# Optimization experiments

Measured on AMD Instinct MI355X. Metric: run time of the kernel, lower is better.

## Reference

```python
import jax, jax.numpy as jnp
import numpy as np
import math

B, S, D, H, DH, R = 2, 2048, 1024, 16, 64, 8
EPS = 1e-5


def setup_inputs() -> dict:
    key = jax.random.key(0)
    ks = jax.random.split(key, 8)
    hidden_states = jax.random.normal(ks[0], (B, S, D), jnp.float32)
    # causal boolean mask (batch, seq, seq); every row has >=1 valid entry
    causal = jnp.tril(jnp.ones((S, S), dtype=bool))
    attention_mask = jnp.broadcast_to(causal, (B, S, S))
    # lora: (n_layers=1, 4, batch, hidden, rank); [0]=qA,[1]=kA,[2]=qB,[3]=kB
    lora = jax.random.normal(ks[1], (1, 4, B, D, R), jnp.float32) * 0.02
    ln_w = jnp.ones((D,), jnp.float32)
    Wq = jax.random.normal(ks[2], (D, D), jnp.float32) * 0.02
    Wk = jax.random.normal(ks[3], (D, D), jnp.float32) * 0.02
    Wv = jax.random.normal(ks[4], (D, D), jnp.float32) * 0.02
    Wo = jax.random.normal(ks[5], (D, D), jnp.float32) * 0.02
    return dict(hidden_states=hidden_states, attention_mask=attention_mask,
                lora=lora, ln_w=ln_w, Wq=Wq, Wk=Wk, Wv=Wv, Wo=Wo)


def _rms_ln(x, w):
    # model_center LayerNorm with bias=False == RMS layernorm
    var = jnp.mean(x * x, axis=-1, keepdims=True)
    return x * jax.lax.rsqrt(var + EPS) * w


def _lora_delta(h, A, Bm):
    # h: (b,s,D), A: (b,D,R), Bm: (b,R,D);  h + (h@A)@Bm * 2
    z = jnp.einsum('bsd,bdr->bsr', h, A)
    return h + jnp.einsum('bsr,brd->bsd', z, Bm) * 2


def reference(hidden_states, attention_mask, lora, ln_w, Wq, Wk, Wv, Wo):
    b, s, _ = hidden_states.shape
    x = _rms_ln(hidden_states, ln_w)
    h_q = x @ Wq.T
    h_k = x @ Wk.T
    h_v = x @ Wv.T
    layer = lora[0]  # (4, b, D, R)
    h_q = _lora_delta(h_q, layer[0], jnp.swapaxes(layer[2], 1, 2))
    h_k = _lora_delta(h_k, layer[1], jnp.swapaxes(layer[3], 1, 2))
    q = h_q.reshape(b, s, H, DH)
    k = h_k.reshape(b, s, H, DH)
    v = h_v.reshape(b, s, H, DH)
    score = jnp.einsum('bqhd,bkhd->bhqk', q, k) / math.sqrt(DH)
    m = attention_mask[:, None, :, :]  # (b,1,s,s)
    score = jnp.where(m, score, -jnp.inf)
    p = jax.nn.softmax(score, axis=-1)
    p = jnp.where(m, p, jnp.float32(0))
    out = jnp.einsum('bhqk,bkhd->bqhd', p, v).reshape(b, s, H * DH)
    out = out @ Wo.T
    return hidden_states + out
```

## Files before the change

kernel.cpp:

```cpp
#include <hip/hip_runtime.h>

typedef __bf16 bf16;
typedef __bf16 bf16x4 __attribute__((ext_vector_type(4)));
typedef __bf16 bf16x8 __attribute__((ext_vector_type(8)));
typedef float f32x4 __attribute__((ext_vector_type(4)));

#define DM 1024
#define NROW 4096
#define SEQ 2048
#define HDIM 64
#define NEGBIG -30000.0f

#define SWB(base, row, bcol) \
  ((char*)(base) + (row) * 128 + ((bcol) ^ (((row) & 7) << 4)))

__device__ __forceinline__ void async16(const bf16* g, bf16* l) {
  __builtin_amdgcn_global_load_lds(
      (const __attribute__((address_space(1))) unsigned int*)g,
      (__attribute__((address_space(3))) unsigned int*)l, 16, 0, 0);
}

template <bool F32OUT>
__device__ __forceinline__ void gemm128(const bf16* __restrict__ A,
                                        const bf16* __restrict__ Bw,
                                        bf16* __restrict__ Cb,
                                        float* __restrict__ Cf,
                                        const float* __restrict__ resid,
                                        int m0, int n0) {
  __shared__ __align__(16) bf16 sA[128 * 32];
  __shared__ __align__(16) bf16 sB[128 * 32];
  const int t = threadIdx.x;
  const int lane = t & 63;
  const int w = t >> 6;
  const int wm = (w & 1) * 64;
  const int wn = (w >> 1) * 64;
  const int lr = lane & 15;
  const int kg = lane >> 4;

  f32x4 acc[4][4];
#pragma unroll
  for (int i = 0; i < 4; i++)
#pragma unroll
    for (int j = 0; j < 4; j++)
#pragma unroll
      for (int r = 0; r < 4; r++) acc[i][j][r] = 0.0f;

  const int srow = t >> 2;
  const int scol = (t & 3) * 8;
  const bf16* gA = A + (size_t)(m0 + srow) * DM + scol;
  const bf16* gB = Bw + (size_t)(n0 + srow) * DM + scol;
  bf16* lA = &sA[t * 8];
  bf16* lB = &sB[t * 8];

  for (int k0 = 0; k0 < DM; k0 += 32) {
    async16(gA + k0, lA);
    async16(gA + k0 + 64 * DM, lA + 2048);
    async16(gB + k0, lB);
    async16(gB + k0 + 64 * DM, lB + 2048);
    __syncthreads();
    bf16x8 av[4], bv[4];
#pragma unroll
    for (int mi = 0; mi < 4; mi++)
      av[mi] = *(const bf16x8*)&sA[(wm + mi * 16 + lr) * 32 + kg * 8];
#pragma unroll
    for (int nj = 0; nj < 4; nj++)
      bv[nj] = *(const bf16x8*)&sB[(wn + nj * 16 + lr) * 32 + kg * 8];
#pragma unroll
    for (int mi = 0; mi < 4; mi++)
#pragma unroll
      for (int nj = 0; nj < 4; nj++)
        acc[mi][nj] = __builtin_amdgcn_mfma_f32_16x16x32_bf16(av[mi], bv[nj],
                                                              acc[mi][nj], 0, 0, 0);
    __syncthreads();
  }

#pragma unroll
  for (int mi = 0; mi < 4; mi++) {
#pragma unroll
    for (int r = 0; r < 4; r++) {
      const int grow = m0 + wm + mi * 16 + kg * 4 + r;
      const size_t base = (size_t)grow * DM + n0 + wn + lr;
#pragma unroll
      for (int nj = 0; nj < 4; nj++) {
        float v = acc[mi][nj][r];
        if (F32OUT) {
          Cf[base + nj * 16] = v + resid[base + nj * 16];
        } else {
          Cb[base + nj * 16] = (bf16)v;
        }
      }
    }
  }
}

__global__ __launch_bounds__(256) void k_cast4(const float* __restrict__ a,
                                               const float* __restrict__ b,
                                               const float* __restrict__ c,
                                               const float* __restrict__ e,
                                               bf16* __restrict__ d) {
  const int i = blockIdx.x * 256 + threadIdx.x;
  const int mat = i >> 18;
  const int off = i & 262143;
  const float* s = (mat == 0) ? a : (mat == 1) ? b : (mat == 2) ? c : e;
  const float4 v = ((const float4*)s)[off];
  bf16x4 o;
  o[0] = (bf16)v.x; o[1] = (bf16)v.y; o[2] = (bf16)v.z; o[3] = (bf16)v.w;
  ((bf16x4*)d)[i] = o;
}

__global__ __launch_bounds__(256) void k_rmsnorm(const float* __restrict__ hin,
                                                 const float* __restrict__ wln,
                                                 bf16* __restrict__ xo) {
  const int row = blockIdx.x;
  const int t = threadIdx.x;
  const float4 h4 = ((const float4*)(hin + (size_t)row * DM))[t];
  float ss = h4.x * h4.x + h4.y * h4.y + h4.z * h4.z + h4.w * h4.w;
#pragma unroll
  for (int off = 1; off < 64; off <<= 1) ss += __shfl_xor(ss, off, 64);
  __shared__ float red[4];
  if ((t & 63) == 0) red[t >> 6] = ss;
  __syncthreads();
  ss = red[0] + red[1] + red[2] + red[3];
  const float inv = rsqrtf(ss * (1.0f / DM) + 1e-5f);
  const float4 w4 = ((const float4*)wln)[t];
  bf16x4 o;
  o[0] = (bf16)(h4.x * inv * w4.x);
  o[1] = (bf16)(h4.y * inv * w4.y);
  o[2] = (bf16)(h4.z * inv * w4.z);
  o[3] = (bf16)(h4.w * inv * w4.w);
  *(bf16x4*)&xo[(size_t)row * DM + t * 4] = o;
}

__global__ __launch_bounds__(256) void k_qkv(const bf16* __restrict__ x,
                                             const bf16* __restrict__ Wq,
                                             const bf16* __restrict__ Wk,
                                             const bf16* __restrict__ Wv,
                                             bf16* __restrict__ hq,
                                             bf16* __restrict__ hk,
                                             bf16* __restrict__ hv) {
  const int nb = blockIdx.y;
  const int wsel = nb >> 3;
  const int n0 = (nb & 7) * 128;
  const bf16* Bw = (wsel == 0) ? Wq : (wsel == 1) ? Wk : Wv;
  bf16* C = (wsel == 0) ? hq : (wsel == 1) ? hk : hv;
  gemm128<false>(x, Bw, C, nullptr, nullptr, blockIdx.x * 128, n0);
}

__global__ __launch_bounds__(256) void k_oproj(const bf16* __restrict__ ctx,
                                               const bf16* __restrict__ Wo,
                                               const float* __restrict__ resid,
                                               float* __restrict__ out) {
  gemm128<true>(ctx, Wo, nullptr, out, resid, blockIdx.x * 128, blockIdx.y * 128);
}

__global__ __launch_bounds__(256) void k_vt(const bf16* __restrict__ hv,
                                            bf16* __restrict__ hvT) {
  __shared__ __align__(16) bf16 sT[64 * 64];
  const int t = threadIdx.x;
  const int s0 = blockIdx.x * 64;
  const int c0 = blockIdx.y * 64;
  const int b = blockIdx.z;
  const int r = t >> 2;
  const int cc = (t & 3) * 16;
  const bf16* g = hv + ((size_t)(b * SEQ + s0 + r)) * DM + c0 + cc;
  const bf16x8 a0 = *(const bf16x8*)g;
  const bf16x8 a1 = *(const bf16x8*)(g + 8);
  *(bf16x8*)SWB(sT, r, cc * 2) = a0;
  *(bf16x8*)SWB(sT, r, cc * 2 + 16) = a1;
  __syncthreads();
  bf16x8 o0, o1;
#pragma unroll
  for (int j = 0; j < 8; j++) {
    o0[j] = *(const bf16*)SWB(sT, cc + j, r * 2);
    o1[j] = *(const bf16*)SWB(sT, cc + 8 + j, r * 2);
  }
  bf16* o = hvT + ((size_t)(b * DM + c0 + r)) * SEQ + s0 + cc;
  *(bf16x8*)o = o0;
  *(bf16x8*)(o + 8) = o1;
}

__global__ __launch_bounds__(256) void k_lora2(bf16* __restrict__ hq,
                                               bf16* __restrict__ hk,
                                               const float* __restrict__ lora) {
  const int row0 = blockIdx.x * 32;
  const int which = blockIdx.y;
  const int b = row0 >> 11;
  bf16* H = (which == 0 ? hq : hk) + (size_t)row0 * DM;
  const float* Am = lora + (size_t)(which == 0 ? 0 : 1) * 16384 + (size_t)b * 8192;
  const float* Bm = lora + (size_t)(which == 0 ? 2 : 3) * 16384 + (size_t)b * 8192;
  const int t = threadIdx.x;
  const int lane = t & 63;
  const int w = t >> 6;
  const int lr = lane & 15;
  const int kg = lane >> 4;

  __shared__ __align__(16) bf16 At[8 * 1024];
  __shared__ float Zp[2][32][8];

  const int d0 = lane * 16;
  float4 Bv[32];
  {
    const float4* bp = (const float4*)(Bm + (size_t)d0 * 8);
#pragma unroll
    for (int i = 0; i < 32; i++) Bv[i] = bp[i];
  }

  {
    const float4* ap = (const float4*)(Am + (size_t)t * 32);
#pragma unroll
    for (int i = 0; i < 8; i++) {
      const float4 v = ap[i];
      const int idx = t * 32 + i * 4;
      At[(idx & 7) * 1024 + (idx >> 3)]             = (bf16)v.x;
      At[((idx + 1) & 7) * 1024 + ((idx + 1) >> 3)] = (bf16)v.y;
      At[((idx + 2) & 7) * 1024 + ((idx + 2) >> 3)] = (bf16)v.z;
      At[((idx + 3) & 7) * 1024 + ((idx + 3) >> 3)] = (bf16)v.w;
    }
  }
  __syncthreads();

  const int tile = w & 1;
  const int khalf = w >> 1;
  {
    f32x4 zacc;
#pragma unroll
    for (int r = 0; r < 4; r++) zacc[r] = 0.f;
    const bf16* gH = H + (size_t)(tile * 16 + lr) * DM + khalf * 512 + kg * 8;
    const bf16* lA = &At[(lr & 7) * 1024 + khalf * 512 + kg * 8];
#pragma unroll
    for (int i = 0; i < 16; i++) {
      const bf16x8 ah = *(const bf16x8*)(gH + i * 32);
      const bf16x8 ba = *(const bf16x8*)(lA + i * 32);
      zacc = __builtin_amdgcn_mfma_f32_16x16x32_bf16(ah, ba, zacc, 0, 0, 0);
    }
    if (lr < 8) {
#pragma unroll
      for (int r = 0; r < 4; r++) Zp[khalf][tile * 16 + kg * 4 + r][lr] = zacc[r];
    }
  }
  __syncthreads();

#pragma unroll
  for (int rr = 0; rr < 8; rr++) {
    const int row = w * 8 + rr;
    const float4 z0 = *(const float4*)&Zp[0][row][0];
    const float4 z1 = *(const float4*)&Zp[0][row][4];
    const float4 y0 = *(const float4*)&Zp[1][row][0];
    const float4 y1 = *(const float4*)&Zp[1][row][4];
    const float za = z0.x + y0.x, zb = z0.y + y0.y, zc = z0.z + y0.z, zd = z0.w + y0.w;
    const float ze = z1.x + y1.x, zf = z1.y + y1.y, zg = z1.z + y1.z, zh = z1.w + y1.w;
    bf16* hp = H + (size_t)row * DM + d0;
    const bf16x8 h0 = *(const bf16x8*)hp;
    const bf16x8 h1 = *(const bf16x8*)(hp + 8);
    bf16x8 o0, o1;
#pragma unroll
    for (int j = 0; j < 16; j++) {
      const float4 b0 = Bv[2 * j];
      const float4 b1 = Bv[2 * j + 1];
      const float delta = za * b0.x + zb * b0.y + zc * b0.z + zd * b0.w +
                          ze * b1.x + zf * b1.y + zg * b1.z + zh * b1.w;
      const float hj = (j < 8) ? (float)h0[j] : (float)h1[j - 8];
      const bf16 ov = (bf16)(hj + 2.0f * delta);
      if (j < 8) o0[j] = ov; else o1[j - 8] = ov;
    }
    *(bf16x8*)hp = o0;
    *(bf16x8*)(hp + 8) = o1;
  }
}

__global__ __launch_bounds__(256, 4) void k_attn(const bf16* __restrict__ hq,
                                                 const bf16* __restrict__ hk,
                                                 const bf16* __restrict__ hvT,
                                                 bf16* __restrict__ ctx) {
  const int n = blockIdx.x;
  const int slab = n & 31;
  const int hh = slab & 15;
  const int b = slab >> 4;
  const int xx = n >> 5;
  const int s = xx >> 3;
  const int v = xx & 7;
  const int qt = (s == 0) ? 4 * v : (s == 1) ? 31 - 4 * v
               : (s == 2) ? 4 * v + 2 : 29 - 4 * v;
  const int qbase = qt * 64;

  const int t = threadIdx.x;
  const int lane = t & 63;
  const int w = t >> 6;
  const int lr = lane & 15;
  const int kg = lane >> 4;

  __shared__ __align__(16) bf16 sQ[64 * 64];
  __shared__ __align__(16) bf16 sK[64 * 64];
  __shared__ __align__(16) bf16 sVt[64 * 64];
  __shared__ __align__(16) bf16 sP[64 * 64];

  const size_t rowbase = (size_t)b * SEQ;
  const int hoff = hh * HDIM;
  const float sscale = 0.18033688011112042f;

  const int r4 = t >> 2;
  const int ce = (t & 3) * 16;
  const int cb = (t & 3) * 32;

  {
    const bf16* g = hq + (rowbase + qbase + r4) * DM + hoff + ce;
    bf16x8 q0 = *(const bf16x8*)g;
    bf16x8 q1 = *(const bf16x8*)(g + 8);
    bf16x8 o0, o1;
#pragma unroll
    for (int j = 0; j < 8; j++) {
      o0[j] = (bf16)((float)q0[j] * sscale);
      o1[j] = (bf16)((float)q1[j] * sscale);
    }
    *(bf16x8*)SWB(sQ, r4, cb) = o0;
    *(bf16x8*)SWB(sQ, r4, cb + 16) = o1;
  }

  const bf16* gK = hk + (rowbase + r4) * DM + hoff + ce;
  const bf16* gV = hvT + ((size_t)slab * HDIM + r4) * SEQ + ce;
  bf16x8 kr0 = *(const bf16x8*)gK;
  bf16x8 kr1 = *(const bf16x8*)(gK + 8);
  bf16x8 vr0 = *(const bf16x8*)gV;
  bf16x8 vr1 = *(const bf16x8*)(gV + 8);

  float m_l = NEGBIG, l_l = 0.f;
  f32x4 oacc[4];
#pragma unroll
  for (int nj = 0; nj < 4; nj++)
#pragma unroll
    for (int r = 0; r < 4; r++) oacc[nj][r] = 0.f;

  __syncthreads();

  for (int kt = 0; kt <= qt; kt++) {
    *(bf16x8*)SWB(sK, r4, cb) = kr0;
    *(bf16x8*)SWB(sK, r4, cb + 16) = kr1;
    *(bf16x8*)SWB(sVt, r4, cb) = vr0;
    *(bf16x8*)SWB(sVt, r4, cb + 16) = vr1;
    __syncthreads();

    if (kt < qt) {
      const bf16* gK2 = gK + (size_t)(kt + 1) * 64 * DM;
      const bf16* gV2 = gV + (kt + 1) * 64;
      kr0 = *(const bf16x8*)gK2;
      kr1 = *(const bf16x8*)(gK2 + 8);
      vr0 = *(const bf16x8*)gV2;
      vr1 = *(const bf16x8*)(gV2 + 8);
    }

    f32x4 sc[4];
#pragma unroll
    for (int nj = 0; nj < 4; nj++)
#pragma unroll
      for (int r = 0; r < 4; r++) sc[nj][r] = 0.f;
#pragma unroll
    for (int ks = 0; ks < 2; ks++) {
      const bf16x8 bq = *(const bf16x8*)SWB(sQ, w * 16 + lr, ks * 64 + kg * 16);
#pragma unroll
      for (int nj = 0; nj < 4; nj++) {
        const bf16x8 ak = *(const bf16x8*)SWB(sK, nj * 16 + lr, ks * 64 + kg * 16);
        sc[nj] = __builtin_amdgcn_mfma_f32_16x16x32_bf16(ak, bq, sc[nj], 0, 0, 0);
      }
    }

    if (kt == qt) {
      const int ql = w * 16 + lr;
#pragma unroll
      for (int nj = 0; nj < 4; nj++)
#pragma unroll
        for (int r = 0; r < 4; r++) {
          const int kl = nj * 16 + kg * 4 + r;
          sc[nj][r] = (kl <= ql) ? sc[nj][r] : NEGBIG;
        }
    }

    float rm = sc[0][0];
#pragma unroll
    for (int nj = 0; nj < 4; nj++)
#pragma unroll
      for (int r = 0; r < 4; r++) rm = fmaxf(rm, sc[nj][r]);
    rm = fmaxf(rm, __shfl_xor(rm, 16, 64));
    rm = fmaxf(rm, __shfl_xor(rm, 32, 64));
    const float mnew = fmaxf(m_l, rm);
    const float alpha = __builtin_amdgcn_exp2f(m_l - mnew);
    float rs = 0.f;
#pragma unroll
    for (int nj = 0; nj < 4; nj++)
#pragma unroll
      for (int r = 0; r < 4; r++) {
        const float p = __builtin_amdgcn_exp2f(sc[nj][r] - mnew);
        sc[nj][r] = p;
        rs += p;
      }
    rs += __shfl_xor(rs, 16, 64);
    rs += __shfl_xor(rs, 32, 64);
    l_l = l_l * alpha + rs;
    m_l = mnew;

#pragma unroll
    for (int nj = 0; nj < 4; nj++) {
      bf16x4 p4;
#pragma unroll
      for (int r = 0; r < 4; r++) p4[r] = (bf16)sc[nj][r];
      *(bf16x4*)SWB(sP, w * 16 + lr, nj * 32 + kg * 8) = p4;
    }

#pragma unroll
    for (int r = 0; r < 4; r++) {
      const float ar = __shfl(alpha, (lane & 48) | (kg * 4 + r), 64);
#pragma unroll
      for (int nj = 0; nj < 4; nj++) oacc[nj][r] *= ar;
    }

#pragma unroll
    for (int ks = 0; ks < 2; ks++) {
      const bf16x8 ap = *(const bf16x8*)SWB(sP, w * 16 + lr, ks * 64 + kg * 16);
#pragma unroll
      for (int nj = 0; nj < 4; nj++) {
        const bf16x8 bv = *(const bf16x8*)SWB(sVt, nj * 16 + lr, ks * 64 + kg * 16);
        oacc[nj] = __builtin_amdgcn_mfma_f32_16x16x32_bf16(ap, bv, oacc[nj], 0, 0, 0);
      }
    }
    __syncthreads();
  }

#pragma unroll
  for (int r = 0; r < 4; r++) {
    const float lrow = __shfl(l_l, (lane & 48) | (kg * 4 + r), 64);
    const float invl = 1.0f / lrow;
    const int qr = qbase + w * 16 + kg * 4 + r;
    const size_t base = (rowbase + qr) * DM + hoff + lr;
#pragma unroll
    for (int nj = 0; nj < 4; nj++)
      ctx[base + nj * 16] = (bf16)(oacc[nj][r] * invl);
  }
}

extern "C" void kernel_launch(void* const* d_in, const int* in_sizes, int n_in,
                              void* d_out, int out_size, void* d_ws, size_t ws_size,
                              hipStream_t stream) {
  const float* hidden = (const float*)d_in[0];
  const float* lora = (const float*)d_in[2];
  const float* wln  = (const float*)d_in[3];
  const float* Wq   = (const float*)d_in[4];
  const float* Wk   = (const float*)d_in[5];
  const float* Wv   = (const float*)d_in[6];
  const float* Wo   = (const float*)d_in[7];
  float* out = (float*)d_out;

  const size_t BUF = (size_t)NROW * DM;
  if (ws_size < 4 * BUF * sizeof(bf16)) return;
  bf16* ws = (bf16*)d_ws;
  bf16* hq  = ws;
  bf16* hk  = ws + 1 * BUF;
  bf16* hv  = ws + 2 * BUF;
  bf16* ctx = ws + 3 * BUF;

  bf16* dob = (bf16*)d_out;
  bf16* x   = dob;
  bf16* wqb = dob + BUF;
  bf16* wkb = dob + BUF + DM * DM;
  bf16* wvb = dob + BUF + 2 * DM * DM;
  bf16* wob = dob + BUF + 3 * DM * DM;
  bf16* hvT = dob;

  k_cast4<<<dim3(4 * 1024), dim3(256), 0, stream>>>(Wq, Wk, Wv, Wo, wqb);
  k_rmsnorm<<<dim3(NROW), dim3(256), 0, stream>>>(hidden, wln, x);
  k_qkv<<<dim3(32, 24), dim3(256), 0, stream>>>(x, wqb, wkb, wvb, hq, hk, hv);
  k_vt<<<dim3(SEQ / 64, DM / 64, 2), dim3(256), 0, stream>>>(hv, hvT);
  k_lora2<<<dim3(128, 2), dim3(256), 0, stream>>>(hq, hk, lora);
  k_attn<<<dim3(1024), dim3(256), 0, stream>>>(hq, hk, hvT, ctx);
  k_oproj<<<dim3(32, 8), dim3(256), 0, stream>>>(ctx, wob, hidden, out);
}
```

Measured before the change: 222.0 us.

## Merge small kernels and double-buffer attention K/V with async LDS loads

Merges the weight-cast and RMSnorm kernels into one launch, and the V-transpose and LoRA kernels into another, cutting launch count and tail gaps. In the attention kernel, K and V tiles are now double-buffered in LDS and fetched with global_load_lds async copies issued one tile ahead, in place of the register staging and extra LDS store pass. MFMA sections are wrapped in s_setprio, and the launch-bounds occupancy hint drops from 4 to 3 to make room for the larger LDS footprint. The async loads use an XOR-swizzled layout that has to match the SWB read pattern, and the extra LDS per block may lower occupancy.

Measured after the change: 226.8 us. +2.2%, slower.

```diff
diff --git a/kernel.cpp b/kernel.cpp
--- a/kernel.cpp
+++ b/kernel.cpp
@@ -93,42 +93,44 @@
   }
 }
 
-__global__ __launch_bounds__(256) void k_cast4(const float* __restrict__ a,
-                                               const float* __restrict__ b,
-                                               const float* __restrict__ c,
-                                               const float* __restrict__ e,
-                                               bf16* __restrict__ d) {
-  const int i = blockIdx.x * 256 + threadIdx.x;
-  const int mat = i >> 18;
-  const int off = i & 262143;
-  const float* s = (mat == 0) ? a : (mat == 1) ? b : (mat == 2) ? c : e;
-  const float4 v = ((const float4*)s)[off];
-  bf16x4 o;
-  o[0] = (bf16)v.x; o[1] = (bf16)v.y; o[2] = (bf16)v.z; o[3] = (bf16)v.w;
-  ((bf16x4*)d)[i] = o;
-}
-
-__global__ __launch_bounds__(256) void k_rmsnorm(const float* __restrict__ hin,
-                                                 const float* __restrict__ wln,
-                                                 bf16* __restrict__ xo) {
-  const int row = blockIdx.x;
+__global__ __launch_bounds__(256) void k_pre(const float* __restrict__ hin,
+                                             const float* __restrict__ wln,
+                                             const float* __restrict__ Wq,
+                                             const float* __restrict__ Wk,
+                                             const float* __restrict__ Wv,
+                                             const float* __restrict__ Wo,
+                                             bf16* __restrict__ xo,
+                                             bf16* __restrict__ wcast) {
+  __shared__ float red[4];
   const int t = threadIdx.x;
-  const float4 h4 = ((const float4*)(hin + (size_t)row * DM))[t];
-  float ss = h4.x * h4.x + h4.y * h4.y + h4.z * h4.z + h4.w * h4.w;
-#pragma unroll
-  for (int off = 1; off < 64; off <<= 1) ss += __shfl_xor(ss, off, 64);
-  __shared__ float red[4];
-  if ((t & 63) == 0) red[t >> 6] = ss;
-  __syncthreads();
-  ss = red[0] + red[1] + red[2] + red[3];
-  const float inv = rsqrtf(ss * (1.0f / DM) + 1e-5f);
-  const float4 w4 = ((const float4*)wln)[t];
-  bf16x4 o;
-  o[0] = (bf16)(h4.x * inv * w4.x);
-  o[1] = (bf16)(h4.y * inv * w4.y);
-  o[2] = (bf16)(h4.z * inv * w4.z);
-  o[3] = (bf16)(h4.w * inv * w4.w);
-  *(bf16x4*)&xo[(size_t)row * DM + t * 4] = o;
+  const int bb = blockIdx.x;
+  if (bb < NROW) {
+    const int row = bb;
+    const float4 h4 = ((const float4*)(hin + (size_t)row * DM))[t];
+    float ss = h4.x * h4.x + h4.y * h4.y + h4.z * h4.z + h4.w * h4.w;
+#pragma unroll
+    for (int off = 1; off < 64; off <<= 1) ss += __shfl_xor(ss, off, 64);
+    if ((t & 63) == 0) red[t >> 6] = ss;
+    __syncthreads();
+    ss = red[0] + red[1] + red[2] + red[3];
+    const float inv = rsqrtf(ss * (1.0f / DM) + 1e-5f);
+    const float4 w4 = ((const float4*)wln)[t];
+    bf16x4 o;
+    o[0] = (bf16)(h4.x * inv * w4.x);
+    o[1] = (bf16)(h4.y * inv * w4.y);
+    o[2] = (bf16)(h4.z * inv * w4.z);
+    o[3] = (bf16)(h4.w * inv * w4.w);
+    *(bf16x4*)&xo[(size_t)row * DM + t * 4] = o;
+  } else {
+    const int i = (bb - NROW) * 256 + t;
+    const int mat = i >> 18;
+    const int off = i & 262143;
+    const float* s = (mat == 0) ? Wq : (mat == 1) ? Wk : (mat == 2) ? Wv : Wo;
+    const float4 v = ((const float4*)s)[off];
+    bf16x4 o;
+    o[0] = (bf16)v.x; o[1] = (bf16)v.y; o[2] = (bf16)v.z; o[3] = (bf16)v.w;
+    ((bf16x4*)wcast)[i] = o;
+  }
 }
 
 __global__ __launch_bounds__(256) void k_qkv(const bf16* __restrict__ x,
@@ -153,122 +155,126 @@
   gemm128<true>(ctx, Wo, nullptr, out, resid, blockIdx.x * 128, blockIdx.y * 128);
 }
 
-__global__ __launch_bounds__(256) void k_vt(const bf16* __restrict__ hv,
-                                            bf16* __restrict__ hvT) {
-  __shared__ __align__(16) bf16 sT[64 * 64];
+__global__ __launch_bounds__(256) void k_mid(const bf16* __restrict__ hv,
+                                             bf16* __restrict__ hvT,
+                                             bf16* __restrict__ hq,
+                                             bf16* __restrict__ hk,
+                                             const float* __restrict__ lora) {
+  __shared__ __align__(16) char smem[18432];
   const int t = threadIdx.x;
-  const int s0 = blockIdx.x * 64;
-  const int c0 = blockIdx.y * 64;
-  const int b = blockIdx.z;
-  const int r = t >> 2;
-  const int cc = (t & 3) * 16;
-  const bf16* g = hv + ((size_t)(b * SEQ + s0 + r)) * DM + c0 + cc;
-  const bf16x8 a0 = *(const bf16x8*)g;
-  const bf16x8 a1 = *(const bf16x8*)(g + 8);
-  *(bf16x8*)SWB(sT, r, cc * 2) = a0;
-  *(bf16x8*)SWB(sT, r, cc * 2 + 16) = a1;
-  __syncthreads();
-  bf16x8 o0, o1;
-#pragma unroll
-  for (int j = 0; j < 8; j++) {
-    o0[j] = *(const bf16*)SWB(sT, cc + j, r * 2);
-    o1[j] = *(const bf16*)SWB(sT, cc + 8 + j, r * 2);
-  }
-  bf16* o = hvT + ((size_t)(b * DM + c0 + r)) * SEQ + s0 + cc;
-  *(bf16x8*)o = o0;
-  *(bf16x8*)(o + 8) = o1;
-}
-
-__global__ __launch_bounds__(256) void k_lora2(bf16* __restrict__ hq,
-                                               bf16* __restrict__ hk,
-                                               const float* __restrict__ lora) {
-  const int row0 = blockIdx.x * 32;
-  const int which = blockIdx.y;
-  const int b = row0 >> 11;
-  bf16* H = (which == 0 ? hq : hk) + (size_t)row0 * DM;
-  const float* Am = lora + (size_t)(which == 0 ? 0 : 1) * 16384 + (size_t)b * 8192;
-  const float* Bm = lora + (size_t)(which == 0 ? 2 : 3) * 16384 + (size_t)b * 8192;
-  const int t = threadIdx.x;
+  const int bb = blockIdx.x;
   const int lane = t & 63;
   const int w = t >> 6;
   const int lr = lane & 15;
   const int kg = lane >> 4;
 
-  __shared__ __align__(16) bf16 At[8 * 1024];
-  __shared__ float Zp[2][32][8];
-
-  const int d0 = lane * 16;
-  float4 Bv[32];
-  {
-    const float4* bp = (const float4*)(Bm + (size_t)d0 * 8);
-#pragma unroll
-    for (int i = 0; i < 32; i++) Bv[i] = bp[i];
-  }
-
-  {
-    const float4* ap = (const float4*)(Am + (size_t)t * 32);
-#pragma unroll
-    for (int i = 0; i < 8; i++) {
-      const float4 v = ap[i];
-      const int idx = t * 32 + i * 4;
-      At[(idx & 7) * 1024 + (idx >> 3)]             = (bf16)v.x;
-      At[((idx + 1) & 7) * 1024 + ((idx + 1) >> 3)] = (bf16)v.y;
-      At[((idx + 2) & 7) * 1024 + ((idx + 2) >> 3)] = (bf16)v.z;
-      At[((idx + 3) & 7) * 1024 + ((idx + 3) >> 3)] = (bf16)v.w;
-    }
-  }
-  __syncthreads();
-
-  const int tile = w & 1;
-  const int khalf = w >> 1;
-  {
-    f32x4 zacc;
-#pragma unroll
-    for (int r = 0; r < 4; r++) zacc[r] = 0.f;
-    const bf16* gH = H + (size_t)(tile * 16 + lr) * DM + khalf * 512 + kg * 8;
-    const bf16* lA = &At[(lr & 7) * 1024 + khalf * 512 + kg * 8];
-#pragma unroll
-    for (int i = 0; i < 16; i++) {
-      const bf16x8 ah = *(const bf16x8*)(gH + i * 32);
-      const bf16x8 ba = *(const bf16x8*)(lA + i * 32);
-      zacc = __builtin_amdgcn_mfma_f32_16x16x32_bf16(ah, ba, zacc, 0, 0, 0);
-    }
-    if (lr < 8) {
-#pragma unroll
-      for (int r = 0; r < 4; r++) Zp[khalf][tile * 16 + kg * 4 + r][lr] = zacc[r];
-    }
-  }
-  __syncthreads();
-
-#pragma unroll
-  for (int rr = 0; rr < 8; rr++) {
-    const int row = w * 8 + rr;
-    const float4 z0 = *(const float4*)&Zp[0][row][0];
-    const float4 z1 = *(const float4*)&Zp[0][row][4];
-    const float4 y0 = *(const float4*)&Zp[1][row][0];
-    const float4 y1 = *(const float4*)&Zp[1][row][4];
-    const float za = z0.x + y0.x, zb = z0.y + y0.y, zc = z0.z + y0.z, zd = z0.w + y0.w;
-    const float ze = z1.x + y1.x, zf = z1.y + y1.y, zg = z1.z + y1.z, zh = z1.w + y1.w;
-    bf16* hp = H + (size_t)row * DM + d0;
-    const bf16x8 h0 = *(const bf16x8*)hp;
-    const bf16x8 h1 = *(const bf16x8*)(hp + 8);
+  if (bb < 1024) {
+    bf16* sT = (bf16*)smem;
+    const int s0 = (bb & 31) * 64;
+    const int c0 = ((bb >> 5) & 15) * 64;
+    const int b = bb >> 9;
+    const int r = t >> 2;
+    const int cc = (t & 3) * 16;
+    const bf16* g = hv + ((size_t)(b * SEQ + s0 + r)) * DM + c0 + cc;
+    const bf16x8 a0 = *(const bf16x8*)g;
+    const bf16x8 a1 = *(const bf16x8*)(g + 8);
+    *(bf16x8*)SWB(sT, r, cc * 2) = a0;
+    *(bf16x8*)SWB(sT, r, cc * 2 + 16) = a1;
+    __syncthreads();
     bf16x8 o0, o1;
 #pragma unroll
-    for (int j = 0; j < 16; j++) {
-      const float4 b0 = Bv[2 * j];
-      const float4 b1 = Bv[2 * j + 1];
-      const float delta = za * b0.x + zb * b0.y + zc * b0.z + zd * b0.w +
-                          ze * b1.x + zf * b1.y + zg * b1.z + zh * b1.w;
-      const float hj = (j < 8) ? (float)h0[j] : (float)h1[j - 8];
-      const bf16 ov = (bf16)(hj + 2.0f * delta);
-      if (j < 8) o0[j] = ov; else o1[j - 8] = ov;
-    }
-    *(bf16x8*)hp = o0;
-    *(bf16x8*)(hp + 8) = o1;
-  }
-}
-
-__global__ __launch_bounds__(256, 4) void k_attn(const bf16* __restrict__ hq,
+    for (int j = 0; j < 8; j++) {
+      o0[j] = *(const bf16*)SWB(sT, cc + j, r * 2);
+      o1[j] = *(const bf16*)SWB(sT, cc + 8 + j, r * 2);
+    }
+    bf16* o = hvT + ((size_t)(b * DM + c0 + r)) * SEQ + s0 + cc;
+    *(bf16x8*)o = o0;
+    *(bf16x8*)(o + 8) = o1;
+  } else {
+    bf16* At = (bf16*)smem;
+    float* Zp = (float*)(smem + 16384);
+    const int lid = bb - 1024;
+    const int row0 = (lid & 127) * 32;
+    const int which = lid >> 7;
+    const int b = row0 >> 11;
+    bf16* H = (which == 0 ? hq : hk) + (size_t)row0 * DM;
+    const float* Am = lora + (size_t)(which == 0 ? 0 : 1) * 16384 + (size_t)b * 8192;
+    const float* Bm = lora + (size_t)(which == 0 ? 2 : 3) * 16384 + (size_t)b * 8192;
+
+    const int d0 = lane * 16;
+    float4 Bv[32];
+    {
+      const float4* bp = (const float4*)(Bm + (size_t)d0 * 8);
+#pragma unroll
+      for (int i = 0; i < 32; i++) Bv[i] = bp[i];
+    }
+
+    {
+      const float4* ap = (const float4*)(Am + (size_t)t * 32);
+#pragma unroll
+      for (int i = 0; i < 8; i++) {
+        const float4 v = ap[i];
+        const int idx = t * 32 + i * 4;
+        At[(idx & 7) * 1024 + (idx >> 3)]             = (bf16)v.x;
+        At[((idx + 1) & 7) * 1024 + ((idx + 1) >> 3)] = (bf16)v.y;
+        At[((idx + 2) & 7) * 1024 + ((idx + 2) >> 3)] = (bf16)v.z;
+        At[((idx + 3) & 7) * 1024 + ((idx + 3) >> 3)] = (bf16)v.w;
+      }
+    }
+    __syncthreads();
+
+    const int tile = w & 1;
+    const int khalf = w >> 1;
+    {
+      f32x4 zacc;
+#pragma unroll
+      for (int r = 0; r < 4; r++) zacc[r] = 0.f;
+      const bf16* gH = H + (size_t)(tile * 16 + lr) * DM + khalf * 512 + kg * 8;
+      const bf16* lA = &At[(lr & 7) * 1024 + khalf * 512 + kg * 8];
+#pragma unroll
+      for (int i = 0; i < 16; i++) {
+        const bf16x8 ah = *(const bf16x8*)(gH + i * 32);
+        const bf16x8 ba = *(const bf16x8*)(lA + i * 32);
+        zacc = __builtin_amdgcn_mfma_f32_16x16x32_bf16(ah, ba, zacc, 0, 0, 0);
+      }
+      if (lr < 8) {
+#pragma unroll
+        for (int r = 0; r < 4; r++)
+          Zp[(khalf * 32 + tile * 16 + kg * 4 + r) * 8 + lr] = zacc[r];
+      }
+    }
+    __syncthreads();
+
+#pragma unroll
+    for (int rr = 0; rr < 8; rr++) {
+      const int row = w * 8 + rr;
+      const float4 z0 = *(const float4*)&Zp[(row) * 8 + 0];
+      const float4 z1 = *(const float4*)&Zp[(row) * 8 + 4];
+      const float4 y0 = *(const float4*)&Zp[(32 + row) * 8 + 0];
+      const float4 y1 = *(const float4*)&Zp[(32 + row) * 8 + 4];
+      const float za = z0.x + y0.x, zb = z0.y + y0.y, zc = z0.z + y0.z, zd = z0.w + y0.w;
+      const float ze = z1.x + y1.x, zf = z1.y + y1.y, zg = z1.z + y1.z, zh = z1.w + y1.w;
+      bf16* hp = H + (size_t)row * DM + d0;
+      const bf16x8 h0 = *(const bf16x8*)hp;
+      const bf16x8 h1 = *(const bf16x8*)(hp + 8);
+      bf16x8 o0, o1;
+#pragma unroll
+      for (int j = 0; j < 16; j++) {
+        const float4 b0 = Bv[2 * j];
+        const float4 b1 = Bv[2 * j + 1];
+        const float delta = za * b0.x + zb * b0.y + zc * b0.z + zd * b0.w +
+                            ze * b1.x + zf * b1.y + zg * b1.z + zh * b1.w;
+        const float hj = (j < 8) ? (float)h0[j] : (float)h1[j - 8];
+        const bf16 ov = (bf16)(hj + 2.0f * delta);
+        if (j < 8) o0[j] = ov; else o1[j - 8] = ov;
+      }
+      *(bf16x8*)hp = o0;
+      *(bf16x8*)(hp + 8) = o1;
+    }
+  }
+}
+
+__global__ __launch_bounds__(256, 3) void k_attn(const bf16* __restrict__ hq,
                                                  const bf16* __restrict__ hk,
                                                  const bf16* __restrict__ hvT,
                                                  bf16* __restrict__ ctx) {
@@ -290,19 +296,18 @@
   const int kg = lane >> 4;
 
   __shared__ __align__(16) bf16 sQ[64 * 64];
-  __shared__ __align__(16) bf16 sK[64 * 64];
-  __shared__ __align__(16) bf16 sVt[64 * 64];
+  __shared__ __align__(16) bf16 sK[2][64 * 64];
+  __shared__ __align__(16) bf16 sVt[2][64 * 64];
   __shared__ __align__(16) bf16 sP[64 * 64];
 
   const size_t rowbase = (size_t)b * SEQ;
   const int hoff = hh * HDIM;
   const float sscale = 0.18033688011112042f;
 
-  const int r4 = t >> 2;
-  const int ce = (t & 3) * 16;
-  const int cb = (t & 3) * 32;
-
   {
+    const int r4 = t >> 2;
+    const int ce = (t & 3) * 16;
+    const int cb = (t & 3) * 32;
     const bf16* g = hq + (rowbase + qbase + r4) * DM + hoff + ce;
     bf16x8 q0 = *(const bf16x8*)g;
     bf16x8 q1 = *(const bf16x8*)(g + 8);
@@ -316,12 +321,27 @@
     *(bf16x8*)SWB(sQ, r4, cb + 16) = o1;
   }
 
-  const bf16* gK = hk + (rowbase + r4) * DM + hoff + ce;
-  const bf16* gV = hvT + ((size_t)slab * HDIM + r4) * SEQ + ce;
-  bf16x8 kr0 = *(const bf16x8*)gK;
-  bf16x8 kr1 = *(const bf16x8*)(gK + 8);
-  bf16x8 vr0 = *(const bf16x8*)gV;
-  bf16x8 vr1 = *(const bf16x8*)(gV + 8);
+  const int l3 = lane >> 3;
+  const int dcol = ((lane & 7) ^ l3) * 8;
+  const int drow = w * 16 + l3;
+  const bf16* gKb = hk + (rowbase + drow) * DM + hoff + dcol;
+  const bf16* gVb = hvT + ((size_t)slab * HDIM + drow) * SEQ + dcol;
+  bf16* lK = &sK[0][0] + w * 1024 + lane * 8;
+  bf16* lV = &sVt[0][0] + w * 1024 + lane * 8;
+
+#define ISSUE_KV(kt_, buf_)                                          \
+  {                                                                  \
+    const bf16* gk_ = gKb + (size_t)(kt_) * 64 * DM;                 \
+    const bf16* gv_ = gVb + (kt_) * 64;                              \
+    bf16* lk_ = lK + (buf_) * 4096;                                  \
+    bf16* lv_ = lV + (buf_) * 4096;                                  \
+    async16(gk_, lk_);                                               \
+    async16(gk_ + 8 * DM, lk_ + 512);                                \
+    async16(gv_, lv_);                                               \
+    async16(gv_ + 8 * SEQ, lv_ + 512);                               \
+  }
+
+  ISSUE_KV(0, 0);
 
   float m_l = NEGBIG, l_l = 0.f;
   f32x4 oacc[4];
@@ -330,38 +350,31 @@
 #pragma unroll
     for (int r = 0; r < 4; r++) oacc[nj][r] = 0.f;
 
+  asm volatile("s_waitcnt vmcnt(0)" ::: "memory");
   __syncthreads();
 
   for (int kt = 0; kt <= qt; kt++) {
-    *(bf16x8*)SWB(sK, r4, cb) = kr0;
-    *(bf16x8*)SWB(sK, r4, cb + 16) = kr1;
-    *(bf16x8*)SWB(sVt, r4, cb) = vr0;
-    *(bf16x8*)SWB(sVt, r4, cb + 16) = vr1;
-    __syncthreads();
-
-    if (kt < qt) {
-      const bf16* gK2 = gK + (size_t)(kt + 1) * 64 * DM;
-      const bf16* gV2 = gV + (kt + 1) * 64;
-      kr0 = *(const bf16x8*)gK2;
-      kr1 = *(const bf16x8*)(gK2 + 8);
-      vr0 = *(const bf16x8*)gV2;
-      vr1 = *(const bf16x8*)(gV2 + 8);
-    }
+    const int cur = kt & 1;
+    if (kt < qt) ISSUE_KV(kt + 1, cur ^ 1);
+    const bf16* sKc = &sK[cur][0];
+    const bf16* sVc = &sVt[cur][0];
 
     f32x4 sc[4];
 #pragma unroll
     for (int nj = 0; nj < 4; nj++)
 #pragma unroll
       for (int r = 0; r < 4; r++) sc[nj][r] = 0.f;
+    __builtin_amdgcn_s_setprio(1);
 #pragma unroll
     for (int ks = 0; ks < 2; ks++) {
       const bf16x8 bq = *(const bf16x8*)SWB(sQ, w * 16 + lr, ks * 64 + kg * 16);
 #pragma unroll
       for (int nj = 0; nj < 4; nj++) {
-        const bf16x8 ak = *(const bf16x8*)SWB(sK, nj * 16 + lr, ks * 64 + kg * 16);
+        const bf16x8 ak = *(const bf16x8*)SWB(sKc, nj * 16 + lr, ks * 64 + kg * 16);
         sc[nj] = __builtin_amdgcn_mfma_f32_16x16x32_bf16(ak, bq, sc[nj], 0, 0, 0);
       }
     }
+    __builtin_amdgcn_s_setprio(0);
 
     if (kt == qt) {
       const int ql = w * 16 + lr;
@@ -412,15 +425,19 @@
       for (int nj = 0; nj < 4; nj++) oacc[nj][r] *= ar;
     }
 
+    __builtin_amdgcn_s_setprio(1);
 #pragma unroll
     for (int ks = 0; ks < 2; ks++) {
       const bf16x8 ap = *(const bf16x8*)SWB(sP, w * 16 + lr, ks * 64 + kg * 16);
 #pragma unroll
       for (int nj = 0; nj < 4; nj++) {
-        const bf16x8 bv = *(const bf16x8*)SWB(sVt, nj * 16 + lr, ks * 64 + kg * 16);
+        const bf16x8 bv = *(const bf16x8*)SWB(sVc, nj * 16 + lr, ks * 64 + kg * 16);
         oacc[nj] = __builtin_amdgcn_mfma_f32_16x16x32_bf16(ap, bv, oacc[nj], 0, 0, 0);
       }
     }
+    __builtin_amdgcn_s_setprio(0);
+
+    asm volatile("s_waitcnt vmcnt(0)" ::: "memory");
     __syncthreads();
   }
 
@@ -464,11 +481,9 @@
   bf16* wob = dob + BUF + 3 * DM * DM;
   bf16* hvT = dob;
 
-  k_cast4<<<dim3(4 * 1024), dim3(256), 0, stream>>>(Wq, Wk, Wv, Wo, wqb);
-  k_rmsnorm<<<dim3(NROW), dim3(256), 0, stream>>>(hidden, wln, x);
+  k_pre<<<dim3(2 * NROW), dim3(256), 0, stream>>>(hidden, wln, Wq, Wk, Wv, Wo, x, wqb);
   k_qkv<<<dim3(32, 24), dim3(256), 0, stream>>>(x, wqb, wkb, wvb, hq, hk, hv);
-  k_vt<<<dim3(SEQ / 64, DM / 64, 2), dim3(256), 0, stream>>>(hv, hvT);
-  k_lora2<<<dim3(128, 2), dim3(256), 0, stream>>>(hq, hk, lora);
+  k_mid<<<dim3(1280), dim3(256), 0, stream>>>(hv, hvT, hq, hk, lora);
   k_attn<<<dim3(1024), dim3(256), 0, stream>>>(hq, hk, hvT, ctx);
   k_oproj<<<dim3(32, 8), dim3(256), 0, stream>>>(ctx, wob, hidden, out);
 }
```
